# Optimization experiments

Measured on AMD Instinct MI355X. Metric: run time of the kernel, lower is better.

The kernel has to match this reference:

```python
import jax, jax.numpy as jnp
import numpy as np
import math

D_MODEL = 1024
N_HEADS = 16
HEAD_DIM = D_MODEL // N_HEADS
THETA = 10000.0


def _rope(x, cos, sin):
    # x: [b, h, s, head_dim]; cos/sin: [s, head_dim//2]
    xe = x[..., 0::2]
    xo = x[..., 1::2]
    re = xe * cos - xo * sin
    ro = xe * sin + xo * cos
    # interleave back to even/odd layout
    return jnp.stack([re, ro], axis=-1).reshape(x.shape)


def setup_inputs() -> dict:
    key = jax.random.key(0)
    k1, k2, k3, k4, k5 = jax.random.split(key, 5)
    std = math.sqrt(2.0 / (D_MODEL + D_MODEL))
    x = jax.random.normal(k1, (2, 2048, D_MODEL), dtype=jnp.float32)
    Wq = jax.random.normal(k2, (D_MODEL, D_MODEL), dtype=jnp.float32) * std
    Wk = jax.random.normal(k3, (D_MODEL, D_MODEL), dtype=jnp.float32) * std
    Wv = jax.random.normal(k4, (D_MODEL, D_MODEL), dtype=jnp.float32) * std
    Wo = jax.random.normal(k5, (D_MODEL, D_MODEL), dtype=jnp.float32) * (std / math.sqrt(2))
    return {"x": x, "Wq": Wq, "Wk": Wk, "Wv": Wv, "Wo": Wo}


def reference(x, Wq, Wk, Wv, Wo):
    b, s, d = x.shape
    h, hd = N_HEADS, HEAD_DIM
    # projections: einsum 'batch seq d_in, d_model d_in -> batch seq d_model' == x @ W.T
    def proj(W):
        y = jnp.einsum('bsd,md->bsm', x, W)
        return y.reshape(b, s, h, hd).transpose(0, 2, 1, 3)  # [b, h, s, hd]
    Q, K, V = proj(Wq), proj(Wk), proj(Wv)
    # RoPE with default positions = arange(seq)
    freqs = 1.0 / (THETA ** (jnp.arange(0, hd, 2, dtype=jnp.float32) / hd))
    angles = jnp.arange(s, dtype=jnp.float32)[:, None] * freqs[None, :]  # [s, hd//2]
    cos, sin = jnp.cos(angles), jnp.sin(angles)
    Q = _rope(Q, cos, sin)
    K = _rope(K, cos, sin)
    # naive causal attention
    scores = jnp.einsum('bhqd,bhkd->bhqk', Q, K) / math.sqrt(hd)
    causal = jnp.tril(jnp.ones((s, s), dtype=bool))
    scores = jnp.where(causal, scores, -jnp.inf)
    attn = jax.nn.softmax(scores, axis=-1)
    out = jnp.einsum('bhqk,bhkd->bhqd', attn, V)
    out = out.transpose(0, 2, 1, 3).reshape(b, s, d)
    return jnp.einsum('bsd,md->bsm', out, Wo)
```

## Files before the change

### kernel.cpp

```cpp
#include <hip/hip_runtime.h>
#include <stdint.h>
#include <stddef.h>

typedef __bf16 bf16;
typedef __bf16 bf16x8 __attribute__((ext_vector_type(8)));
typedef __bf16 bf16x4 __attribute__((ext_vector_type(4)));
typedef short short4v __attribute__((ext_vector_type(4)));
typedef float f32x4 __attribute__((ext_vector_type(4)));

#define GAS __attribute__((address_space(1)))
#define LAS __attribute__((address_space(3)))

__device__ __forceinline__ void async_load16(const void* g, void* l) {
  __builtin_amdgcn_global_load_lds((const GAS void*)g, (LAS void*)l, 16, 0, 0);
}

__device__ __forceinline__ f32x4 mfma16(bf16x4 a, bf16x4 b, f32x4 c) {
#if defined(__HIP_DEVICE_COMPILE__)
#if __has_builtin(__builtin_amdgcn_mfma_f32_16x16x16bf16_1k)
  return __builtin_amdgcn_mfma_f32_16x16x16bf16_1k(
      __builtin_bit_cast(short4v, a), __builtin_bit_cast(short4v, b), c, 0, 0, 0);
#else
  f32x4 d;
  asm volatile("v_mfma_f32_16x16x16_bf16 %0, %1, %2, %3"
               : "=v"(d)
               : "v"(a), "v"(b), "v"(c));
  return d;
#endif
#else
  (void)a; (void)b;
  return c;
#endif
}

__global__ __launch_bounds__(256) void cast_all(
    const float* __restrict__ x, const float* __restrict__ Wq,
    const float* __restrict__ Wk, const float* __restrict__ Wv,
    const float* __restrict__ Wo, bf16* __restrict__ Xh,
    bf16* __restrict__ Wqkv, bf16* __restrict__ Woh) {
  int idx = (blockIdx.x * 256 + threadIdx.x) * 4;
  const float* src;
  bf16* dst;
  float scale = 1.0f;
  if (idx < 4194304) {
    src = x + idx; dst = Xh + idx;
  } else if (idx < 7340032) {
    int j = idx - 4194304;
    if (j < 1048576) {
      src = Wq + j; scale = 0.18033688011112042f;
    } else {
      src = ((j < 2097152) ? Wk : Wv) + (j & 1048575);
    }
    dst = Wqkv + j;
  } else {
    int j = idx - 7340032;
    src = Wo + j; dst = Woh + j;
  }
  float4 v = *(const float4*)src;
  bf16x4 o;
  o[0] = (bf16)(v.x * scale); o[1] = (bf16)(v.y * scale);
  o[2] = (bf16)(v.z * scale); o[3] = (bf16)(v.w * scale);
  *(bf16x4*)dst = o;
}

__global__ __launch_bounds__(256) void gemm_qkv(
    const bf16* __restrict__ A, const bf16* __restrict__ B,
    bf16* __restrict__ Qh, bf16* __restrict__ Kh, bf16* __restrict__ Vt,
    int K) {
  __shared__ __align__(16) bf16 As[128 * 32];
  __shared__ __align__(16) bf16 Bs[128 * 32];
  const int tid = threadIdx.x;
  const int wave = tid >> 6, lane = tid & 63;
  const int bm = blockIdx.y * 128, bn = blockIdx.x * 128;
  const int wm = (wave >> 1) * 64, wn = (wave & 1) * 64;
  const int lrow = lane >> 2, lk = (lane & 3) * 8;
  const int fr = lane & 15, fk = (lane >> 4) * 8;

  f32x4 acc[4][4] = {};

  for (int kt = 0; kt < K; kt += 32) {
    __syncthreads();
#pragma unroll
    for (int c = 0; c < 2; ++c) {
      const int chunk = wave * 2 + c;
      const bf16* ga = A + (size_t)(bm + chunk * 16 + lrow) * K + kt + lk;
      async_load16(ga, (void*)(As + chunk * 512));
      const bf16* gb = B + (size_t)(bn + chunk * 16 + lrow) * K + kt + lk;
      async_load16(gb, (void*)(Bs + chunk * 512));
    }
    __syncthreads();

    bf16x8 af[4], bfr[4];
#pragma unroll
    for (int i = 0; i < 4; ++i)
      af[i] = *(const bf16x8*)&As[(wm + i * 16 + fr) * 32 + fk];
#pragma unroll
    for (int j = 0; j < 4; ++j)
      bfr[j] = *(const bf16x8*)&Bs[(wn + j * 16 + fr) * 32 + fk];
#pragma unroll
    for (int i = 0; i < 4; ++i)
#pragma unroll
      for (int j = 0; j < 4; ++j)
        acc[i][j] =
            __builtin_amdgcn_mfma_f32_16x16x32_bf16(af[i], bfr[j], acc[i][j], 0, 0, 0);
  }

  const int r0 = (lane >> 4) * 4, cc = lane & 15;
  const bool oddl = cc & 1;
#pragma unroll
  for (int i = 0; i < 4; ++i) {
    const int row0 = bm + wm + i * 16 + r0;
    const int b = row0 >> 11, s0 = row0 & 2047;
#pragma unroll
    for (int j = 0; j < 4; ++j) {
      const int col = bn + wn + j * 16 + cc;
      if (col < 2048) {
        const int hcol = col & 1023;
        const int h = hcol >> 6, d = hcol & 63;
        const int ip = d >> 1;
        const float freq = __expf((float)ip * -0.2878231366242557f);
        bf16* dst = (col < 1024 ? Qh : Kh) + ((size_t)(b * 16 + h) * 2048) * 64 + d;
#pragma unroll
        for (int r = 0; r < 4; ++r) {
          float own = acc[i][j][r];
          float oth = __shfl_xor(own, 1, 64);
          float sn, cs;
          __sincosf((float)(s0 + r) * freq, &sn, &cs);
          float res = oddl ? (oth * sn + own * cs) : (own * cs - oth * sn);
          dst[(size_t)(s0 + r) * 64] = (bf16)res;
        }
      } else {
        const int v = col - 2048, h = v >> 6, d = v & 63;
        bf16x4 o;
#pragma unroll
        for (int r = 0; r < 4; ++r) o[r] = (bf16)acc[i][j][r];
        *(bf16x4*)&Vt[(((size_t)b * 16 + h) * 64 + d) * 2048 + s0] = o;
      }
    }
  }
}

template <typename OutT, int BM, int BN>
__global__ __launch_bounds__(256) void gemm_bt(
    const bf16* __restrict__ A, const bf16* __restrict__ B,
    OutT* __restrict__ C, int M, int N, int K) {
  constexpr int ACH = BM / 16, NCH = (BM + BN) / 16, PW = NCH / 4;
  constexpr int FM = BM / 32, FN = BN / 32;
  __shared__ __align__(16) bf16 As[BM * 32];
  __shared__ __align__(16) bf16 Bs[BN * 32];
  const int tid = threadIdx.x;
  const int wave = tid >> 6, lane = tid & 63;
  const int bm = blockIdx.y * BM, bn = blockIdx.x * BN;
  const int wm = (wave >> 1) * (BM / 2), wn = (wave & 1) * (BN / 2);
  const int lrow = lane >> 2, lk = (lane & 3) * 8;
  const int fr = lane & 15, fk = (lane >> 4) * 8;

  f32x4 acc[FM][FN] = {};

  for (int kt = 0; kt < K; kt += 32) {
    __syncthreads();
#pragma unroll
    for (int c = 0; c < PW; ++c) {
      const int chunk = wave * PW + c;
      if (chunk < ACH) {
        const bf16* ga = A + (size_t)(bm + chunk * 16 + lrow) * K + kt + lk;
        async_load16(ga, (void*)(As + chunk * 512));
      } else {
        const int bc = chunk - ACH;
        const bf16* gb = B + (size_t)(bn + bc * 16 + lrow) * K + kt + lk;
        async_load16(gb, (void*)(Bs + bc * 512));
      }
    }
    __syncthreads();

    bf16x8 af[FM], bfr[FN];
#pragma unroll
    for (int i = 0; i < FM; ++i)
      af[i] = *(const bf16x8*)&As[(wm + i * 16 + fr) * 32 + fk];
#pragma unroll
    for (int j = 0; j < FN; ++j)
      bfr[j] = *(const bf16x8*)&Bs[(wn + j * 16 + fr) * 32 + fk];
#pragma unroll
    for (int i = 0; i < FM; ++i)
#pragma unroll
      for (int j = 0; j < FN; ++j)
        acc[i][j] =
            __builtin_amdgcn_mfma_f32_16x16x32_bf16(af[i], bfr[j], acc[i][j], 0, 0, 0);
  }

  const int r0 = (lane >> 4) * 4, cc = lane & 15;
#pragma unroll
  for (int i = 0; i < FM; ++i)
#pragma unroll
    for (int j = 0; j < FN; ++j)
#pragma unroll
      for (int r = 0; r < 4; ++r)
        C[(size_t)(bm + wm + i * 16 + r0 + r) * N + (bn + wn + j * 16 + cc)] =
            (OutT)acc[i][j][r];
}

__global__ __launch_bounds__(128, 2) void attn(const bf16* __restrict__ Qh,
                                               const bf16* __restrict__ Kh,
                                               const bf16* __restrict__ Vt,
                                               bf16* __restrict__ Oh) {
  __shared__ __align__(16) bf16 Vs[2][64 * 72];
  __shared__ float scratch[68 * 64];
  const int f = blockIdx.x;
  const int qt = 31 - (f >> 5);
  const int bh = f & 31;
  const int tid = threadIdx.x, w = tid >> 6, lane = tid & 63;
  const int nlo = lane & 15, g = lane >> 4;
  const int q0 = qt * 64;
  const bf16* __restrict__ Qp = Qh + (size_t)bh * 131072;
  const bf16* __restrict__ Kp = Kh + (size_t)bh * 131072;
  const bf16* __restrict__ Vp = Vt + (size_t)bh * 131072;
  const int n = qt + 1;
  const int hf = (n + 1) >> 1;
  const int t0 = w ? hf : 0;
  const int cnt = w ? (n - hf) : hf;

  bf16x8 aq[4][2];
#pragma unroll
  for (int qb = 0; qb < 4; ++qb)
#pragma unroll
    for (int ks = 0; ks < 2; ++ks)
      aq[qb][ks] =
          *(const bf16x8*)&Qp[(size_t)(q0 + qb * 16 + nlo) * 64 + ks * 32 + g * 8];

  f32x4 oacc[4][4] = {};
  float lsum[4] = {0.f, 0.f, 0.f, 0.f};

  const int srow = lane >> 3, soff = (lane & 7) * 8;
  bf16* __restrict__ Vw = Vs[w];

  bf16x8 pv[8];
  if (cnt > 0) {
#pragma unroll
    for (int c = 0; c < 8; ++c)
      pv[c] = *(const bf16x8*)&Vp[(size_t)(c * 8 + srow) * 2048 + t0 * 64 + soff];
  }

  for (int it = 0; it < cnt; ++it) {
    const int i = t0 + it, kbase = i * 64;
    bf16x8 pk[4][2];
#pragma unroll
    for (int ni = 0; ni < 4; ++ni)
#pragma unroll
      for (int ks = 0; ks < 2; ++ks)
        pk[ni][ks] = *(const bf16x8*)&Kp[(size_t)(kbase + ni * 16 + nlo) * 64 +
                                         ks * 32 + g * 8];
#pragma unroll
    for (int c = 0; c < 8; ++c)
      *(bf16x8*)&Vw[(c * 8 + srow) * 72 + soff] = pv[c];
    if (it + 1 < cnt) {
      const int kb2 = kbase + 64;
#pragma unroll
      for (int c = 0; c < 8; ++c)
        pv[c] = *(const bf16x8*)&Vp[(size_t)(c * 8 + srow) * 2048 + kb2 + soff];
    }

    const bool dg = (i == n - 1);
    bf16x4 p[4][4];
#pragma unroll
    for (int qb = 0; qb < 4; ++qb) {
      f32x4 st[4] = {};
#pragma unroll
      for (int ks = 0; ks < 2; ++ks)
#pragma unroll
        for (int ni = 0; ni < 4; ++ni)
          st[ni] = __builtin_amdgcn_mfma_f32_16x16x32_bf16(pk[ni][ks], aq[qb][ks],
                                                           st[ni], 0, 0, 0);
      const int qg = q0 + qb * 16 + nlo;
#pragma unroll
      for (int ni = 0; ni < 4; ++ni) {
        const int kg0 = kbase + ni * 16 + g * 4;
#pragma unroll
        for (int r = 0; r < 4; ++r) {
          float e = __builtin_amdgcn_exp2f(st[ni][r]);
          e = (!dg || (kg0 + r <= qg)) ? e : 0.0f;
          lsum[qb] += e;
          p[qb][ni][r] = (bf16)e;
        }
      }
    }

#pragma unroll
    for (int ni = 0; ni < 4; ++ni)
#pragma unroll
      for (int mi = 0; mi < 4; ++mi) {
        bf16x4 av = *(const bf16x4*)&Vw[(mi * 16 + nlo) * 72 + ni * 16 + g * 4];
#pragma unroll
        for (int qb = 0; qb < 4; ++qb)
          oacc[qb][mi] = mfma16(av, p[qb][ni], oacc[qb][mi]);
      }
  }

#pragma unroll
  for (int qb = 0; qb < 4; ++qb) {
    lsum[qb] += __shfl_xor(lsum[qb], 16, 64);
    lsum[qb] += __shfl_xor(lsum[qb], 32, 64);
  }

  if (w == 1) {
#pragma unroll
    for (int qb = 0; qb < 4; ++qb) {
#pragma unroll
      for (int mi = 0; mi < 4; ++mi)
#pragma unroll
        for (int r = 0; r < 4; ++r)
          scratch[(qb * 16 + mi * 4 + r) * 64 + lane] = oacc[qb][mi][r];
      scratch[(64 + qb) * 64 + lane] = lsum[qb];
    }
  }
  __syncthreads();
  if (w == 0) {
    const int b = bh >> 4, hd = bh & 15;
#pragma unroll
    for (int qb = 0; qb < 4; ++qb) {
      const float l = lsum[qb] + scratch[(64 + qb) * 64 + lane];
      const float inv = 1.0f / l;
      const int q = q0 + qb * 16 + nlo;
#pragma unroll
      for (int mi = 0; mi < 4; ++mi) {
        bf16x4 o;
#pragma unroll
        for (int r = 0; r < 4; ++r)
          o[r] = (bf16)((oacc[qb][mi][r] +
                         scratch[(qb * 16 + mi * 4 + r) * 64 + lane]) * inv);
        *(bf16x4*)&Oh[((size_t)b * 2048 + q) * 1024 + hd * 64 + mi * 16 + g * 4] = o;
      }
    }
  }
}

extern "C" void kernel_launch(void* const* d_in, const int* in_sizes, int n_in,
                              void* d_out, int out_size, void* d_ws, size_t ws_size,
                              hipStream_t stream) {
  (void)in_sizes; (void)n_in; (void)out_size; (void)ws_size;
  const float* x = (const float*)d_in[0];
  const float* Wq = (const float*)d_in[1];
  const float* Wk = (const float*)d_in[2];
  const float* Wv = (const float*)d_in[3];
  const float* Wo = (const float*)d_in[4];
  float* out = (float*)d_out;
  char* ws = (char*)d_ws;

  bf16* Xh   = (bf16*)(ws);
  bf16* Wqkv = (bf16*)(ws + 8388608);
  bf16* Woh  = (bf16*)(ws + 14680064);
  bf16* Qh   = (bf16*)(ws + 16777216);
  bf16* Kh   = (bf16*)(ws + 25165824);
  bf16* Vt   = (bf16*)(ws + 33554432);
  bf16* Oh   = (bf16*)(ws + 41943040);

  cast_all<<<8192, 256, 0, stream>>>(x, Wq, Wk, Wv, Wo, Xh, Wqkv, Woh);
  gemm_qkv<<<dim3(24, 32), 256, 0, stream>>>(Xh, Wqkv, Qh, Kh, Vt, 1024);
  attn<<<1024, 128, 0, stream>>>(Qh, Kh, Vt, Oh);
  gemm_bt<float, 128, 128><<<dim3(8, 32), 256, 0, stream>>>(Oh, Woh, out, 4096, 1024, 1024);
}
```

Measured before the change: 194.8 us.

## Halve attention query tile and stream V into LDS with async swizzled loads

The attention kernel now handles 32 query rows per block instead of 64 and launches twice as many blocks, with launch bounds raised to 3 blocks per CU. V tiles are copied straight from global memory into LDS with global_load_lds, replacing the register staging path. To avoid LDS bank conflicts without padding, the QKV GEMM writes V^T with an XOR swizzle that the attention reads undo. The causal mask is applied only on the diagonal tile, and the V buffer and reduction scratch share one LDS array. The smaller tile is meant to improve occupancy and load balance, at the cost of loading each K/V tile twice as often across the grid.

```diff
diff --git a/kernel.cpp b/kernel.cpp
--- a/kernel.cpp
+++ b/kernel.cpp
@@ -134,7 +134,8 @@
         bf16x4 o;
 #pragma unroll
         for (int r = 0; r < 4; ++r) o[r] = (bf16)acc[i][j][r];
-        *(bf16x4*)&Vt[(((size_t)b * 16 + h) * 64 + d) * 2048 + s0] = o;
+        const int s2 = (s0 & ~63) | ((s0 ^ ((d & 7) << 3)) & 63);
+        *(bf16x4*)&Vt[(((size_t)b * 16 + h) * 64 + d) * 2048 + s2] = o;
       }
     }
   }
@@ -199,49 +200,50 @@
             (OutT)acc[i][j][r];
 }
 
-__global__ __launch_bounds__(128, 2) void attn(const bf16* __restrict__ Qh,
+__global__ __launch_bounds__(128, 3) void attn(const bf16* __restrict__ Qh,
                                                const bf16* __restrict__ Kh,
                                                const bf16* __restrict__ Vt,
                                                bf16* __restrict__ Oh) {
-  __shared__ __align__(16) bf16 Vs[2][64 * 72];
-  __shared__ float scratch[68 * 64];
+  __shared__ __align__(16) float smem[4096];
+  bf16* __restrict__ Vs = (bf16*)smem;
+  float* __restrict__ scratch = smem;
   const int f = blockIdx.x;
-  const int qt = 31 - (f >> 5);
+  const int j = 63 - (f >> 5);
   const int bh = f & 31;
   const int tid = threadIdx.x, w = tid >> 6, lane = tid & 63;
   const int nlo = lane & 15, g = lane >> 4;
-  const int q0 = qt * 64;
+  const int q0 = j * 32;
   const bf16* __restrict__ Qp = Qh + (size_t)bh * 131072;
   const bf16* __restrict__ Kp = Kh + (size_t)bh * 131072;
   const bf16* __restrict__ Vp = Vt + (size_t)bh * 131072;
-  const int n = qt + 1;
+  const int n = (j >> 1) + 1;
   const int hf = (n + 1) >> 1;
   const int t0 = w ? hf : 0;
   const int cnt = w ? (n - hf) : hf;
 
-  bf16x8 aq[4][2];
-#pragma unroll
-  for (int qb = 0; qb < 4; ++qb)
+  bf16x8 aq[2][2];
+#pragma unroll
+  for (int qb = 0; qb < 2; ++qb)
 #pragma unroll
     for (int ks = 0; ks < 2; ++ks)
       aq[qb][ks] =
           *(const bf16x8*)&Qp[(size_t)(q0 + qb * 16 + nlo) * 64 + ks * 32 + g * 8];
 
-  f32x4 oacc[4][4] = {};
-  float lsum[4] = {0.f, 0.f, 0.f, 0.f};
+  f32x4 oacc[2][4] = {};
+  float lsum[2] = {0.f, 0.f};
 
   const int srow = lane >> 3, soff = (lane & 7) * 8;
-  bf16* __restrict__ Vw = Vs[w];
-
-  bf16x8 pv[8];
-  if (cnt > 0) {
-#pragma unroll
-    for (int c = 0; c < 8; ++c)
-      pv[c] = *(const bf16x8*)&Vp[(size_t)(c * 8 + srow) * 2048 + t0 * 64 + soff];
-  }
+  const int sw = (nlo & 7) << 3;
+  bf16* __restrict__ Vw = Vs + w * 4096;
 
   for (int it = 0; it < cnt; ++it) {
     const int i = t0 + it, kbase = i * 64;
+
+    const bf16* vsrc = Vp + (size_t)srow * 2048 + kbase + soff;
+#pragma unroll
+    for (int c = 0; c < 8; ++c)
+      async_load16(vsrc + (size_t)c * 16384, (void*)(Vw + c * 512));
+
     bf16x8 pk[4][2];
 #pragma unroll
     for (int ni = 0; ni < 4; ++ni)
@@ -249,20 +251,11 @@
       for (int ks = 0; ks < 2; ++ks)
         pk[ni][ks] = *(const bf16x8*)&Kp[(size_t)(kbase + ni * 16 + nlo) * 64 +
                                          ks * 32 + g * 8];
-#pragma unroll
-    for (int c = 0; c < 8; ++c)
-      *(bf16x8*)&Vw[(c * 8 + srow) * 72 + soff] = pv[c];
-    if (it + 1 < cnt) {
-      const int kb2 = kbase + 64;
-#pragma unroll
-      for (int c = 0; c < 8; ++c)
-        pv[c] = *(const bf16x8*)&Vp[(size_t)(c * 8 + srow) * 2048 + kb2 + soff];
-    }
 
     const bool dg = (i == n - 1);
-    bf16x4 p[4][4];
-#pragma unroll
-    for (int qb = 0; qb < 4; ++qb) {
+    bf16x4 p[2][4];
+#pragma unroll
+    for (int qb = 0; qb < 2; ++qb) {
       f32x4 st[4] = {};
 #pragma unroll
       for (int ks = 0; ks < 2; ++ks)
@@ -271,53 +264,68 @@
           st[ni] = __builtin_amdgcn_mfma_f32_16x16x32_bf16(pk[ni][ks], aq[qb][ks],
                                                            st[ni], 0, 0, 0);
       const int qg = q0 + qb * 16 + nlo;
-#pragma unroll
-      for (int ni = 0; ni < 4; ++ni) {
-        const int kg0 = kbase + ni * 16 + g * 4;
-#pragma unroll
-        for (int r = 0; r < 4; ++r) {
-          float e = __builtin_amdgcn_exp2f(st[ni][r]);
-          e = (!dg || (kg0 + r <= qg)) ? e : 0.0f;
-          lsum[qb] += e;
-          p[qb][ni][r] = (bf16)e;
+      if (!dg) {
+#pragma unroll
+        for (int ni = 0; ni < 4; ++ni)
+#pragma unroll
+          for (int r = 0; r < 4; ++r) {
+            float e = __builtin_amdgcn_exp2f(st[ni][r]);
+            lsum[qb] += e;
+            p[qb][ni][r] = (bf16)e;
+          }
+      } else {
+#pragma unroll
+        for (int ni = 0; ni < 4; ++ni) {
+          const int kg0 = kbase + ni * 16 + g * 4;
+#pragma unroll
+          for (int r = 0; r < 4; ++r) {
+            float e = __builtin_amdgcn_exp2f(st[ni][r]);
+            e = (kg0 + r <= qg) ? e : 0.0f;
+            lsum[qb] += e;
+            p[qb][ni][r] = (bf16)e;
+          }
         }
       }
     }
 
+    asm volatile("s_waitcnt vmcnt(0)" ::: "memory");
+
 #pragma unroll
     for (int ni = 0; ni < 4; ++ni)
 #pragma unroll
       for (int mi = 0; mi < 4; ++mi) {
-        bf16x4 av = *(const bf16x4*)&Vw[(mi * 16 + nlo) * 72 + ni * 16 + g * 4];
-#pragma unroll
-        for (int qb = 0; qb < 4; ++qb)
+        bf16x4 av = *(const bf16x4*)&Vw[(mi * 16 + nlo) * 64 +
+                                        ((ni * 16 + g * 4) ^ sw)];
+#pragma unroll
+        for (int qb = 0; qb < 2; ++qb)
           oacc[qb][mi] = mfma16(av, p[qb][ni], oacc[qb][mi]);
       }
   }
 
 #pragma unroll
-  for (int qb = 0; qb < 4; ++qb) {
+  for (int qb = 0; qb < 2; ++qb) {
     lsum[qb] += __shfl_xor(lsum[qb], 16, 64);
     lsum[qb] += __shfl_xor(lsum[qb], 32, 64);
   }
 
+  __syncthreads();
   if (w == 1) {
 #pragma unroll
-    for (int qb = 0; qb < 4; ++qb) {
+    for (int qb = 0; qb < 2; ++qb) {
 #pragma unroll
       for (int mi = 0; mi < 4; ++mi)
 #pragma unroll
         for (int r = 0; r < 4; ++r)
           scratch[(qb * 16 + mi * 4 + r) * 64 + lane] = oacc[qb][mi][r];
-      scratch[(64 + qb) * 64 + lane] = lsum[qb];
+      scratch[(32 + qb) * 64 + lane] = lsum[qb];
     }
   }
   __syncthreads();
   if (w == 0) {
     const int b = bh >> 4, hd = bh & 15;
 #pragma unroll
-    for (int qb = 0; qb < 4; ++qb) {
-      const float l = lsum[qb] + scratch[(64 + qb) * 64 + lane];
+    for (int qb = 0; qb < 2; ++qb) {
+      const float l = lsum[qb] + scratch[(32 + qb) * 64 + lane];
       const float inv = 1.0f / l;
       const int q = q0 + qb * 16 + nlo;
 #pragma unroll
@@ -355,6 +363,6 @@
 
   cast_all<<<8192, 256, 0, stream>>>(x, Wq, Wk, Wv, Wo, Xh, Wqkv, Woh);
   gemm_qkv<<<dim3(24, 32), 256, 0, stream>>>(Xh, Wqkv, Qh, Kh, Vt, 1024);
-  attn<<<1024, 128, 0, stream>>>(Qh, Kh, Vt, Oh);
+  attn<<<2048, 128, 0, stream>>>(Qh, Kh, Vt, Oh);
   gemm_bt<float, 128, 128><<<dim3(8, 32), 256, 0, stream>>>(Oh, Woh, out, 4096, 1024, 1024);
 }
```

Measured after the change: 193.8 us. Within noise of the previous version (-0.5%).
